# Kernel optimization log

Hardware: AMD Instinct MI355X
Metric: run time of the kernel (lower is better)

Reference implementation:

```python
import jax, jax.numpy as jnp
import numpy as np

EPS = 1e-12  # tf/keras l2_normalize epsilon


def _hadamard(n):
    # Sylvester construction; n must be a power of 2
    H = np.array([[1.0]], dtype=np.float32)
    while H.shape[0] < n:
        H = np.block([[H, H], [H, -H]])
    return H


def setup_inputs() -> dict:
    key = jax.random.key(0)
    k1, k2 = jax.random.split(key)
    in_dim, out_dim, batch = 2048, 16384, 1024
    hadamard_size = 16384  # next pow2 of max(in_dim, out_dim)
    H = _hadamard(hadamard_size)[:in_dim, :out_dim]  # [2048, 16384]
    init_scale = 1.0 / np.sqrt(out_dim)
    x = jax.random.normal(k1, (batch, in_dim), dtype=jnp.float32)
    scale = jnp.full((1,), init_scale, dtype=jnp.float32)
    bias = jax.random.uniform(k2, (out_dim,), minval=-init_scale, maxval=init_scale, dtype=jnp.float32)
    return {"x": x, "scale": scale, "bias": bias, "hadamard": jnp.asarray(H)}


def reference(x, scale, bias, hadamard):
    # L2-normalize along features (keras: x / sqrt(max(sum(x^2), eps)))
    sq = jnp.sum(x * x, axis=-1, keepdims=True)
    xn = x * jax.lax.rsqrt(jnp.maximum(sq, EPS))
    # structured Hadamard matmul (expressed as dense GEMM, as in the original)
    out = -scale * jnp.matmul(xn, hadamard)  # [B, out_dim]
    out = out + bias
    return out
```

## Files before the change

### kernel.cpp

```cpp
#include <hip/hip_runtime.h>

#define IN_DIM   2048
#define OUT_DIM  16384
#define NT       256
#define EPS      1e-12f


__device__ __forceinline__ int swz(int e) { return e ^ (((e >> 6) & 7) << 3); }

#define BFLY(m)                                                   \
    _Pragma("unroll")                                             \
    for (int k = 0; k < 8; ++k)                                   \
        if (!(k & (m))) {                                         \
            const float a_ = v[k], b_ = v[k | (m)];               \
            v[k]       = a_ + b_;                                 \
            v[k | (m)] = a_ - b_;                                 \
        }

__global__ __launch_bounds__(NT) void had_fwht_kernel(
    const float* __restrict__ x,
    const float* __restrict__ scale,
    const float* __restrict__ bias,
    float* __restrict__ out)
{
    __shared__ float sA[IN_DIM];
    __shared__ float sB[IN_DIM];
    __shared__ float red[NT / 64];

    const int b = blockIdx.x;
    const int t = threadIdx.x;
    float v[8];

    const float4* xr4 = (const float4*)(x + (size_t)b * IN_DIM);
    const float4 a0 = xr4[2 * t];
    const float4 a1 = xr4[2 * t + 1];
    v[0] = a0.x; v[1] = a0.y; v[2] = a0.z; v[3] = a0.w;
    v[4] = a1.x; v[5] = a1.y; v[6] = a1.z; v[7] = a1.w;

    float local = 0.f;
#pragma unroll
    for (int k = 0; k < 8; ++k) local = fmaf(v[k], v[k], local);
#pragma unroll
    for (int off = 32; off > 0; off >>= 1)
        local += __shfl_down(local, off, 64);
    if ((t & 63) == 0) red[t >> 6] = local;

    BFLY(1) BFLY(2) BFLY(4)
    ((float4*)sA)[swz(8 * t)     >> 2] = make_float4(v[0], v[1], v[2], v[3]);
    ((float4*)sA)[swz(8 * t + 4) >> 2] = make_float4(v[4], v[5], v[6], v[7]);
    __syncthreads();

    const float sumsq = red[0] + red[1] + red[2] + red[3];
    const float c = -scale[0] * rsqrtf(fmaxf(sumsq, EPS));

    {
        const int base = (t & 7) | ((t >> 3) << 6);
#pragma unroll
        for (int k = 0; k < 8; ++k) v[k] = sA[swz(base | (k << 3))];
        BFLY(1) BFLY(2) BFLY(4)
#pragma unroll
        for (int k = 0; k < 8; ++k) sA[swz(base | (k << 3))] = v[k];
    }
    __syncthreads();

    {
        const int base = (t & 63) | ((t >> 6) << 9);
#pragma unroll
        for (int k = 0; k < 8; ++k) v[k] = sA[swz(base | (k << 6))];
        BFLY(1) BFLY(2)
#pragma unroll
        for (int k = 0; k < 8; ++k) sA[swz(base | (k << 6))] = v[k];
    }
    __syncthreads();

#pragma unroll
    for (int k = 0; k < 8; ++k) v[k] = sA[swz(t | (k << 8))];
    BFLY(1) BFLY(2) BFLY(4)
#pragma unroll
    for (int k = 0; k < 8; ++k) sB[t | (k << 8)] = v[k];
    __syncthreads();

    const float4* bias4 = (const float4*)bias;
    const float4* s4    = (const float4*)sB;
    float4* out4        = (float4*)(out + (size_t)b * OUT_DIM);
#pragma unroll
    for (int i = 0; i < OUT_DIM / 4 / NT; ++i) {
        const int idx = t + i * NT;
        const float4 bv = bias4[idx];
        const float4 sv = s4[idx & (IN_DIM / 4 - 1)];
        float4 o;
        o.x = fmaf(c, sv.x, bv.x);
        o.y = fmaf(c, sv.y, bv.y);
        o.z = fmaf(c, sv.z, bv.z);
        o.w = fmaf(c, sv.w, bv.w);
        out4[idx] = o;
    }
}

extern "C" void kernel_launch(void* const* d_in, const int* in_sizes, int n_in,
                              void* d_out, int out_size, void* d_ws, size_t ws_size,
                              hipStream_t stream) {
    const float* x     = (const float*)d_in[0];
    const float* scale = (const float*)d_in[1];
    const float* bias  = (const float*)d_in[2];
    float* out = (float*)d_out;

    const int batch = in_sizes[0] / IN_DIM;
    had_fwht_kernel<<<batch, NT, 0, stream>>>(x, scale, bias, out);
}
```

Before: 18.61 us.

## Process two rows per block, cache bias in registers, drop staging buffer

Each block now handles two batch rows, loading the bias slice once into 16 float4 registers and reusing it for all output tiles of both rows. The final butterfly stage keeps results in registers and writes output directly, which removes the second shared buffer and one barrier. The next row's input is prefetched while the current row's stages run. Register pressure rises, and halving the grid reduces parallelism to 512 blocks. The work is dominated by 64 MB of output writes, so the gain depends on store efficiency more than on compute.

```diff
diff --git a/kernel.cpp b/kernel.cpp
--- a/kernel.cpp
+++ b/kernel.cpp
@@ -3,6 +3,7 @@
 #define IN_DIM   2048
 #define OUT_DIM  16384
 #define NT       256
+#define ROWS     2
 #define EPS      1e-12f
 
 
@@ -17,83 +18,105 @@
             v[k | (m)] = a_ - b_;                                 \
         }
 
-__global__ __launch_bounds__(NT) void had_fwht_kernel(
+__global__ __launch_bounds__(NT, 2) void had_fwht_kernel(
     const float* __restrict__ x,
     const float* __restrict__ scale,
     const float* __restrict__ bias,
     float* __restrict__ out)
 {
-    __shared__ float sA[IN_DIM];
-    __shared__ float sB[IN_DIM];
-    __shared__ float red[NT / 64];
+    __shared__ float sA[ROWS][IN_DIM];
+    __shared__ float red[ROWS][NT / 64];
 
-    const int b = blockIdx.x;
-    const int t = threadIdx.x;
-    float v[8];
+    const int g  = blockIdx.x;
+    const int t  = threadIdx.x;
+    const int wv = t >> 6;
 
-    const float4* xr4 = (const float4*)(x + (size_t)b * IN_DIM);
-    const float4 a0 = xr4[2 * t];
-    const float4 a1 = xr4[2 * t + 1];
-    v[0] = a0.x; v[1] = a0.y; v[2] = a0.z; v[3] = a0.w;
-    v[4] = a1.x; v[5] = a1.y; v[6] = a1.z; v[7] = a1.w;
+    const float negscale = -scale[0];
 
-    float local = 0.f;
+    const float4* bias4 = (const float4*)bias;
+    float4 bj[16];
 #pragma unroll
-    for (int k = 0; k < 8; ++k) local = fmaf(v[k], v[k], local);
+    for (int i = 0; i < 16; ++i)
+        bj[i] = bias4[(i >> 1) * 512 + 2 * t + (i & 1)];
+
+    float p[8];
+    {
+        const float* xr = x + (size_t)(g * ROWS) * IN_DIM;
 #pragma unroll
-    for (int off = 32; off > 0; off >>= 1)
-        local += __shfl_down(local, off, 64);
-    if ((t & 63) == 0) red[t >> 6] = local;
+        for (int k = 0; k < 8; ++k) p[k] = xr[(k << 8) + t];
+    }
 
-    BFLY(1) BFLY(2) BFLY(4)
-    ((float4*)sA)[swz(8 * t)     >> 2] = make_float4(v[0], v[1], v[2], v[3]);
-    ((float4*)sA)[swz(8 * t + 4) >> 2] = make_float4(v[4], v[5], v[6], v[7]);
-    __syncthreads();
+#pragma unroll
+    for (int rr = 0; rr < ROWS; ++rr) {
+        const int row = g * ROWS + rr;
+        float v[8];
+#pragma unroll
+        for (int k = 0; k < 8; ++k) v[k] = p[k];
 
-    const float sumsq = red[0] + red[1] + red[2] + red[3];
-    const float c = -scale[0] * rsqrtf(fmaxf(sumsq, EPS));
+        float local = 0.f;
+#pragma unroll
+        for (int k = 0; k < 8; ++k) local = fmaf(v[k], v[k], local);
+#pragma unroll
+        for (int off = 32; off > 0; off >>= 1)
+            local += __shfl_down(local, off, 64);
+        if ((t & 63) == 0) red[rr][wv] = local;
 
-    {
-        const int base = (t & 7) | ((t >> 3) << 6);
-#pragma unroll
-        for (int k = 0; k < 8; ++k) v[k] = sA[swz(base | (k << 3))];
         BFLY(1) BFLY(2) BFLY(4)
 #pragma unroll
-        for (int k = 0; k < 8; ++k) sA[swz(base | (k << 3))] = v[k];
-    }
-    __syncthreads();
+        for (int k = 0; k < 8; ++k) sA[rr][swz((k << 8) | t)] = v[k];
 
-    {
-        const int base = (t & 63) | ((t >> 6) << 9);
+        if (rr + 1 < ROWS) {
+            const float* xn = x + (size_t)(row + 1) * IN_DIM;
 #pragma unroll
-        for (int k = 0; k < 8; ++k) v[k] = sA[swz(base | (k << 6))];
+            for (int k = 0; k < 8; ++k) p[k] = xn[(k << 8) + t];
+        }
+        __syncthreads();
+
+        const int b1 = ((t >> 3) << 6) | (t & 7);
+#pragma unroll
+        for (int k = 0; k < 8; ++k) v[k] = sA[rr][swz(b1 | (k << 3))];
+        BFLY(1) BFLY(2) BFLY(4)
+#pragma unroll
+        for (int k = 0; k < 8; ++k) sA[rr][swz(b1 | (k << 3))] = v[k];
+        __syncthreads();
+
+        const float sumsq = red[rr][0] + red[rr][1] + red[rr][2] + red[rr][3];
+        const float c = negscale * rsqrtf(fmaxf(sumsq, EPS));
+
+        const int b2 = ((t >> 6) << 8) | (t & 63);
+#pragma unroll
+        for (int k = 0; k < 8; ++k)
+            v[k] = sA[rr][swz(((k >> 2) << 10) | ((k & 3) << 6) | b2)];
         BFLY(1) BFLY(2)
 #pragma unroll
-        for (int k = 0; k < 8; ++k) sA[swz(base | (k << 6))] = v[k];
-    }
-    __syncthreads();
+        for (int k = 0; k < 8; ++k)
+            sA[rr][swz(((k >> 2) << 10) | ((k & 3) << 6) | b2)] = v[k];
+        __syncthreads();
 
+        {
+            const int base = swz(t << 3);
+            const float4 lo = *(const float4*)&sA[rr][base];
+            const float4 hi = *(const float4*)&sA[rr][base + 4];
+            v[0] = lo.x; v[1] = lo.y; v[2] = lo.z; v[3] = lo.w;
+            v[4] = hi.x; v[5] = hi.y; v[6] = hi.z; v[7] = hi.w;
+        }
+        BFLY(1) BFLY(2) BFLY(4)
+
+        float4* orow = (float4*)(out + (size_t)row * OUT_DIM);
 #pragma unroll
-    for (int k = 0; k < 8; ++k) v[k] = sA[swz(t | (k << 8))];
-    BFLY(1) BFLY(2) BFLY(4)
-#pragma unroll
-    for (int k = 0; k < 8; ++k) sB[t | (k << 8)] = v[k];
-    __syncthreads();
-
-    const float4* bias4 = (const float4*)bias;
-    const float4* s4    = (const float4*)sB;
-    float4* out4        = (float4*)(out + (size_t)b * OUT_DIM);
-#pragma unroll
-    for (int i = 0; i < OUT_DIM / 4 / NT; ++i) {
-        const int idx = t + i * NT;
-        const float4 bv = bias4[idx];
-        const float4 sv = s4[idx & (IN_DIM / 4 - 1)];
-        float4 o;
-        o.x = fmaf(c, sv.x, bv.x);
-        o.y = fmaf(c, sv.y, bv.y);
-        o.z = fmaf(c, sv.z, bv.z);
-        o.w = fmaf(c, sv.w, bv.w);
-        out4[idx] = o;
+        for (int tile = 0; tile < 8; ++tile) {
+            float4 o0, o1;
+            o0.x = fmaf(c, v[0], bj[2 * tile].x);
+            o0.y = fmaf(c, v[1], bj[2 * tile].y);
+            o0.z = fmaf(c, v[2], bj[2 * tile].z);
+            o0.w = fmaf(c, v[3], bj[2 * tile].w);
+            o1.x = fmaf(c, v[4], bj[2 * tile + 1].x);
+            o1.y = fmaf(c, v[5], bj[2 * tile + 1].y);
+            o1.z = fmaf(c, v[6], bj[2 * tile + 1].z);
+            o1.w = fmaf(c, v[7], bj[2 * tile + 1].w);
+            orow[tile * 512 + 2 * t]     = o0;
+            orow[tile * 512 + 2 * t + 1] = o1;
+        }
     }
 }
 
@@ -106,5 +129,5 @@
     float* out = (float*)d_out;
 
     const int batch = in_sizes[0] / IN_DIM;
-    had_fwht_kernel<<<batch, NT, 0, stream>>>(x, scale, bias, out);
+    had_fwht_kernel<<<batch / ROWS, NT, 0, stream>>>(x, scale, bias, out);
 }
```

Result: slower. 20.50 us (+10.2%).

## Restructure FWHT to wave-local stages with single barrier and nontemporal stores

Applied to the files above, without the earlier changes.

Reorganizes the butterfly stages so the first three stages stay within each wavefront's 512-element slice, removing intermediate block barriers and leaving one barrier before the last cross-wave stage. That final stage is folded into register math, using each thread's needed sB groups. Bias loads are hoisted to the kernel start to overlap with compute, and outputs are written with nontemporal stores. It also adds a launch-bounds occupancy hint. The risks are higher register pressure from the 16 prefetched bias vectors and reliance on wave-level LDS ordering without explicit intra-wave syncs.

```diff
diff --git a/kernel.cpp b/kernel.cpp
--- a/kernel.cpp
+++ b/kernel.cpp
@@ -4,6 +4,8 @@
 #define OUT_DIM  16384
 #define NT       256
 #define EPS      1e-12f
+
+typedef float f32x4 __attribute__((ext_vector_type(4)));
 
 
 __device__ __forceinline__ int swz(int e) { return e ^ (((e >> 6) & 7) << 3); }
@@ -17,7 +19,7 @@
             v[k | (m)] = a_ - b_;                                 \
         }
 
-__global__ __launch_bounds__(NT) void had_fwht_kernel(
+__global__ __launch_bounds__(NT, 4) void had_fwht_kernel(
     const float* __restrict__ x,
     const float* __restrict__ scale,
     const float* __restrict__ bias,
@@ -29,13 +31,21 @@
 
     const int b = blockIdx.x;
     const int t = threadIdx.x;
-    float v[8];
+    const int l = t & 63;
+    const int w = t >> 6;
 
     const float4* xr4 = (const float4*)(x + (size_t)b * IN_DIM);
     const float4 a0 = xr4[2 * t];
     const float4 a1 = xr4[2 * t + 1];
-    v[0] = a0.x; v[1] = a0.y; v[2] = a0.z; v[3] = a0.w;
-    v[4] = a1.x; v[5] = a1.y; v[6] = a1.z; v[7] = a1.w;
+
+    const float4* bias4 = (const float4*)bias;
+    float4 bj[16];
+#pragma unroll
+    for (int i = 0; i < 16; ++i) bj[i] = bias4[t + i * NT];
+
+    const float negscale = -scale[0];
+
+    float v[8] = {a0.x, a0.y, a0.z, a0.w, a1.x, a1.y, a1.z, a1.w};
 
     float local = 0.f;
 #pragma unroll
@@ -43,57 +53,66 @@
 #pragma unroll
     for (int off = 32; off > 0; off >>= 1)
         local += __shfl_down(local, off, 64);
-    if ((t & 63) == 0) red[t >> 6] = local;
+    if (l == 0) red[w] = local;
 
     BFLY(1) BFLY(2) BFLY(4)
-    ((float4*)sA)[swz(8 * t)     >> 2] = make_float4(v[0], v[1], v[2], v[3]);
-    ((float4*)sA)[swz(8 * t + 4) >> 2] = make_float4(v[4], v[5], v[6], v[7]);
-    __syncthreads();
+
+    {
+        const int base = swz(t << 3);
+        *(float4*)&sA[base]     = make_float4(v[0], v[1], v[2], v[3]);
+        *(float4*)&sA[base + 4] = make_float4(v[4], v[5], v[6], v[7]);
+    }
+    const int bB = (w << 9) | ((l >> 3) << 6) | (l & 7);
+#pragma unroll
+    for (int k = 0; k < 8; ++k) v[k] = sA[swz(bB | (k << 3))];
+    BFLY(1) BFLY(2) BFLY(4)
+
+#pragma unroll
+    for (int k = 0; k < 8; ++k) sA[swz(bB | (k << 3))] = v[k];
+    const int bC = (w << 9) | l;
+#pragma unroll
+    for (int k = 0; k < 8; ++k) v[k] = sA[swz(bC | (k << 6))];
+    BFLY(1) BFLY(2) BFLY(4)
+
+#pragma unroll
+    for (int k = 0; k < 8; ++k) sB[bC | (k << 6)] = v[k];
+
+    asm volatile("s_waitcnt lgkmcnt(0)" ::: "memory");
+    __builtin_amdgcn_s_barrier();
 
     const float sumsq = red[0] + red[1] + red[2] + red[3];
-    const float c = -scale[0] * rsqrtf(fmaxf(sumsq, EPS));
+    const float c = negscale * rsqrtf(fmaxf(sumsq, EPS));
 
-    {
-        const int base = (t & 7) | ((t >> 3) << 6);
+    const float4* sB4 = (const float4*)sB;
+    const int q = t & 127;
+    const float4 G0 = sB4[q];
+    const float4 G1 = sB4[q + 128];
+    const float4 G2 = sB4[q + 256];
+    const float4 G3 = sB4[q + 384];
+
+    float4 s01, d01, s23, d23;
+    s01.x = G0.x + G1.x; s01.y = G0.y + G1.y; s01.z = G0.z + G1.z; s01.w = G0.w + G1.w;
+    d01.x = G0.x - G1.x; d01.y = G0.y - G1.y; d01.z = G0.z - G1.z; d01.w = G0.w - G1.w;
+    s23.x = G2.x + G3.x; s23.y = G2.y + G3.y; s23.z = G2.z + G3.z; s23.w = G2.w + G3.w;
+    d23.x = G2.x - G3.x; d23.y = G2.y - G3.y; d23.z = G2.z - G3.z; d23.w = G2.w - G3.w;
+
+    const bool hi = (t >= 128);
+    const float4 A = hi ? d01 : s01;
+    const float4 B = hi ? d23 : s23;
+    float4 w_e, w_o;
+    w_e.x = A.x + B.x; w_e.y = A.y + B.y; w_e.z = A.z + B.z; w_e.w = A.w + B.w;
+    w_o.x = A.x - B.x; w_o.y = A.y - B.y; w_o.z = A.z - B.z; w_o.w = A.w - B.w;
+
+    f32x4* orow = (f32x4*)(out + (size_t)b * OUT_DIM);
 #pragma unroll
-        for (int k = 0; k < 8; ++k) v[k] = sA[swz(base | (k << 3))];
-        BFLY(1) BFLY(2) BFLY(4)
-#pragma unroll
-        for (int k = 0; k < 8; ++k) sA[swz(base | (k << 3))] = v[k];
-    }
-    __syncthreads();
-
-    {
-        const int base = (t & 63) | ((t >> 6) << 9);
-#pragma unroll
-        for (int k = 0; k < 8; ++k) v[k] = sA[swz(base | (k << 6))];
-        BFLY(1) BFLY(2)
-#pragma unroll
-        for (int k = 0; k < 8; ++k) sA[swz(base | (k << 6))] = v[k];
-    }
-    __syncthreads();
-
-#pragma unroll
-    for (int k = 0; k < 8; ++k) v[k] = sA[swz(t | (k << 8))];
-    BFLY(1) BFLY(2) BFLY(4)
-#pragma unroll
-    for (int k = 0; k < 8; ++k) sB[t | (k << 8)] = v[k];
-    __syncthreads();
-
-    const float4* bias4 = (const float4*)bias;
-    const float4* s4    = (const float4*)sB;
-    float4* out4        = (float4*)(out + (size_t)b * OUT_DIM);
-#pragma unroll
-    for (int i = 0; i < OUT_DIM / 4 / NT; ++i) {
-        const int idx = t + i * NT;
-        const float4 bv = bias4[idx];
-        const float4 sv = s4[idx & (IN_DIM / 4 - 1)];
-        float4 o;
-        o.x = fmaf(c, sv.x, bv.x);
-        o.y = fmaf(c, sv.y, bv.y);
-        o.z = fmaf(c, sv.z, bv.z);
-        o.w = fmaf(c, sv.w, bv.w);
-        out4[idx] = o;
+    for (int i = 0; i < 16; ++i) {
+        const float4 ws = (i & 1) ? w_o : w_e;
+        f32x4 o;
+        o.x = fmaf(c, ws.x, bj[i].x);
+        o.y = fmaf(c, ws.y, bj[i].y);
+        o.z = fmaf(c, ws.z, bj[i].z);
+        o.w = fmaf(c, ws.w, bj[i].w);
+        __builtin_nontemporal_store(o, &orow[t + i * NT]);
     }
 }
 
```

Measured after the change: 17.95 us. 1.04x faster.
